# Performance work log

Measured on AMD Instinct MI355X. Metric: run time of the kernel, lower is better.

Reference implementation:

```python
import jax, jax.numpy as jnp
import numpy as np

B, N, C = 8, 4096, 1024
ATT_DIM = 512
M = 64  # num_outputs


def setup_inputs() -> dict:
    key = jax.random.key(0)
    k_x, k_w, k_b, k_av = jax.random.split(key, 4)
    x = jax.random.normal(k_x, (B, N, C), dtype=jnp.float32)
    # nn.Linear(input_dim, attention_dim): weight (att, C), bias (att,)
    lim = 1.0 / np.sqrt(C)
    W = jax.random.uniform(k_w, (ATT_DIM, C), dtype=jnp.float32, minval=-lim, maxval=lim)
    b = jax.random.uniform(k_b, (ATT_DIM,), dtype=jnp.float32, minval=-lim, maxval=lim)
    # torch.rand -> uniform [0,1)
    attention_vectors = jax.random.uniform(k_av, (M, ATT_DIM), dtype=jnp.float32)
    return {"x": x, "W": W, "b": b, "attention_vectors": attention_vectors}


def reference(x, W, b, attention_vectors):
    # linear projection: (B,N,C) @ (C,att) + bias -> (B,N,att)
    scores = jnp.einsum('bnc,dc->bnd', x, W) + b
    # learned-query attention logits: (B,M,N)
    logits = jnp.einsum('bnd,md->bmn', scores, attention_vectors)
    weights = jax.nn.softmax(logits, axis=-1)
    # pool original features: (B,M,N) @ (B,N,C) -> (B,M,C)
    return jnp.einsum('bmn,bnc->bmc', weights, x)
```

## Files before the change

kernel.cpp:

```cpp
#include <hip/hip_runtime.h>
#include <hip/hip_bf16.h>

#define Bn 8
#define Nn 4096
#define Cn 1024
#define Dn 512
#define Mn 64

typedef __hip_bfloat16 bf16;
typedef __attribute__((ext_vector_type(8))) short short8;
typedef __attribute__((ext_vector_type(4))) short short4x;
typedef __attribute__((ext_vector_type(4))) float f32x4;

#define MFMA16(a, b, c) __builtin_amdgcn_mfma_f32_16x16x32_bf16((a), (b), (c), 0, 0, 0)

__device__ inline short bfbits(float f) {
  union { bf16 b; short s; } u;
  u.b = __float2bfloat16(f);
  return u.s;
}
__device__ inline float bfval(short s) {
  union { short s; bf16 b; } u;
  u.s = s;
  return __bfloat162float(u.b);
}

__global__ __launch_bounds__(256) void prep_kernel(
    const float* __restrict__ W, const float* __restrict__ bias,
    const float* __restrict__ av, bf16* __restrict__ Vhi,
    bf16* __restrict__ Vlo, float* __restrict__ c0) {
  const int m = blockIdx.x;
  const int t = threadIdx.x;
  const int cl = t & 63, dg = t >> 6;
  const int c = blockIdx.y * 64 + cl;
  const float* wp = W + (size_t)(dg * 128) * Cn + c;
  const float* ap = av + m * Dn + dg * 128;
  float a0 = 0.f, a1 = 0.f, a2 = 0.f, a3 = 0.f;
#pragma unroll 8
  for (int i = 0; i < 128; i += 4) {
    a0 = fmaf(ap[i + 0], wp[(size_t)(i + 0) * Cn], a0);
    a1 = fmaf(ap[i + 1], wp[(size_t)(i + 1) * Cn], a1);
    a2 = fmaf(ap[i + 2], wp[(size_t)(i + 2) * Cn], a2);
    a3 = fmaf(ap[i + 3], wp[(size_t)(i + 3) * Cn], a3);
  }
  __shared__ float red[256];
  red[t] = (a0 + a1) + (a2 + a3);
  __syncthreads();
  const float v = red[cl] + red[cl + 64] + red[cl + 128] + red[cl + 192];
  if (dg == 0) {
    const bf16 hi = __float2bfloat16(v);
    Vhi[m * Cn + c] = hi;
    Vlo[m * Cn + c] = __float2bfloat16(v - __bfloat162float(hi));
  }
  if (blockIdx.y == 0) {
    __syncthreads();
    red[t] = av[m * Dn + t] * bias[t] + av[m * Dn + t + 256] * bias[t + 256];
    __syncthreads();
    if (t < 64) {
      float s = red[t] + red[t + 64] + red[t + 128] + red[t + 192];
#pragma unroll
      for (int off = 32; off > 0; off >>= 1) s += __shfl_down(s, off);
      if (t == 0) c0[m] = s;
    }
  }
}

__global__ __launch_bounds__(256, 2) void logits_sm_kernel(
    const float* __restrict__ x, const bf16* __restrict__ Vhi,
    const bf16* __restrict__ Vlo, const float* __restrict__ c0,
    bf16* __restrict__ wgt, float* __restrict__ Mp, float* __restrict__ Sp) {
  const int g = blockIdx.x;
  const int n0 = g * 64;
  const int b = blockIdx.y;
  const int t = threadIdx.x;
  const int w = t >> 6, lane = t & 63, lr = lane & 15, q = lane >> 4;

  const float* xrow = x + (size_t)(b * Nn + n0 + w * 16 + lr) * Cn + q * 8;
  const bf16* vh = Vhi + (size_t)lr * Cn + q * 8;
  const bf16* vl = Vlo + (size_t)lr * Cn + q * 8;

  f32x4 acc[4];
#pragma unroll
  for (int i = 0; i < 4; ++i) acc[i] = (f32x4){0.f, 0.f, 0.f, 0.f};

  float4 xa0[4], xa1[4], xb0[4], xb1[4], xc0[4], xc1[4];
#pragma unroll
  for (int s = 0; s < 4; ++s) {
    xa0[s] = *(const float4*)(xrow + s * 32);
    xa1[s] = *(const float4*)(xrow + s * 32 + 4);
    xb0[s] = *(const float4*)(xrow + 128 + s * 32);
    xb1[s] = *(const float4*)(xrow + 128 + s * 32 + 4);
    xc0[s] = xb0[s]; xc1[s] = xb1[s];
  }

  for (int kc = 0; kc < Cn; kc += 128) {
    if (kc + 256 < Cn) {
#pragma unroll
      for (int s = 0; s < 4; ++s) {
        xc0[s] = *(const float4*)(xrow + kc + 256 + s * 32);
        xc1[s] = *(const float4*)(xrow + kc + 256 + s * 32 + 4);
      }
    }
#pragma unroll
    for (int s = 0; s < 4; ++s) {
      const int kk = kc + s * 32;
      short8 a;
      a[0] = bfbits(xa0[s].x); a[1] = bfbits(xa0[s].y);
      a[2] = bfbits(xa0[s].z); a[3] = bfbits(xa0[s].w);
      a[4] = bfbits(xa1[s].x); a[5] = bfbits(xa1[s].y);
      a[6] = bfbits(xa1[s].z); a[7] = bfbits(xa1[s].w);
#pragma unroll
      for (int mt = 0; mt < 4; ++mt) {
        acc[mt] = MFMA16(a, *(const short8*)(vh + (size_t)(mt * 16) * Cn + kk), acc[mt]);
        acc[mt] = MFMA16(a, *(const short8*)(vl + (size_t)(mt * 16) * Cn + kk), acc[mt]);
      }
    }
#pragma unroll
    for (int s = 0; s < 4; ++s) {
      xa0[s] = xb0[s]; xa1[s] = xb1[s];
      xb0[s] = xc0[s]; xb1[s] = xc1[s];
    }
  }

  __shared__ float wredM[256];
  __shared__ float wredS[256];
  float rmax[4];
#pragma unroll
  for (int mt = 0; mt < 4; ++mt) {
    float r = fmaxf(fmaxf(acc[mt][0], acc[mt][1]), fmaxf(acc[mt][2], acc[mt][3]));
    r = fmaxf(r, __shfl_xor(r, 16));
    r = fmaxf(r, __shfl_xor(r, 32));
    rmax[mt] = r;
  }
  if (q == 0)
#pragma unroll
    for (int mt = 0; mt < 4; ++mt) wredM[w * 64 + mt * 16 + lr] = rmax[mt];
  __syncthreads();
  float vv[4][4];
#pragma unroll
  for (int mt = 0; mt < 4; ++mt) {
    const int m = mt * 16 + lr;
    const float mp = fmaxf(fmaxf(wredM[m], wredM[64 + m]),
                           fmaxf(wredM[128 + m], wredM[192 + m]));
    float s = 0.f;
#pragma unroll
    for (int r = 0; r < 4; ++r) {
      vv[mt][r] = __expf(acc[mt][r] - mp);
      s += vv[mt][r];
    }
    s += __shfl_xor(s, 16);
    s += __shfl_xor(s, 32);
    if (q == 0) wredS[w * 64 + m] = s;
  }
#pragma unroll
  for (int mt = 0; mt < 4; ++mt) {
    const int m = mt * 16 + lr;
    short4x o;
    o[0] = bfbits(vv[mt][0]); o[1] = bfbits(vv[mt][1]);
    o[2] = bfbits(vv[mt][2]); o[3] = bfbits(vv[mt][3]);
    *(short4x*)&wgt[(size_t)(b * Mn + m) * Nn + n0 + w * 16 + q * 4] = o;
  }
  __syncthreads();
  if (w == 0) {
    const int m = lane;
    const float mp = fmaxf(fmaxf(wredM[m], wredM[64 + m]),
                           fmaxf(wredM[128 + m], wredM[192 + m]));
    const float sp = wredS[m] + wredS[64 + m] + wredS[128 + m] + wredS[192 + m];
    Mp[((size_t)b * Mn + m) * 64 + g] = mp + c0[m];
    Sp[((size_t)b * Mn + m) * 64 + g] = sp;
  }
}

__global__ __launch_bounds__(256) void norm_kernel(
    bf16* __restrict__ wgt, const float* __restrict__ Mp,
    const float* __restrict__ Sp) {
  const int row = blockIdx.x;
  const int t = threadIdx.x;
  __shared__ float sMS[2];
  if (t < 64) {
    const float mp = Mp[(size_t)row * 64 + t];
    const float sp = Sp[(size_t)row * 64 + t];
    float M = mp;
#pragma unroll
    for (int off = 32; off > 0; off >>= 1) M = fmaxf(M, __shfl_xor(M, off));
    float e = __expf(mp - M) * sp;
#pragma unroll
    for (int off = 32; off > 0; off >>= 1) e += __shfl_xor(e, off);
    if (t == 0) { sMS[0] = M; sMS[1] = e; }
  }
  __syncthreads();
  const float M = sMS[0], inv = 1.f / sMS[1];
  const float sc = __expf(Mp[(size_t)row * 64 + (t >> 2)] - M) * inv;
  bf16* wp = wgt + (size_t)row * Nn + t * 16;
  short8 u0 = *(const short8*)(wp);
  short8 u1 = *(const short8*)(wp + 8);
  short8 o0, o1;
#pragma unroll
  for (int j = 0; j < 8; ++j) {
    o0[j] = bfbits(bfval(u0[j]) * sc);
    o1[j] = bfbits(bfval(u1[j]) * sc);
  }
  *(short8*)(wp) = o0;
  *(short8*)(wp + 8) = o1;
}

__global__ __launch_bounds__(256, 4) void pool_kernel(
    const float* __restrict__ x, const bf16* __restrict__ wgt,
    float* __restrict__ part) {
  const int cbase = blockIdx.x * 64;
  const int b = blockIdx.y;
  const int ks = blockIdx.z;
  const int t = threadIdx.x;
  __shared__ short XT[2][64][136];
  const int w = t >> 6, lane = t & 63, lr = lane & 15, q = lane >> 4;
  const int mh = (w & 1) * 32, ch = (w >> 1) * 32;
  f32x4 acc[2][2];
#pragma unroll
  for (int i = 0; i < 2; ++i)
#pragma unroll
    for (int j = 0; j < 2; ++j) acc[i][j] = (f32x4){0.f, 0.f, 0.f, 0.f};

  const int h = t & 15, g = t >> 4;
  const int swz = 8 * (h & 7);
  const int swzr0 = 8 * (((ch + lr) >> 2) & 7);
  const int swzr1 = 8 * (((ch + 16 + lr) >> 2) & 7);
  const int NQ = Nn / 8;
  const int kbase = ks * NQ;
  const float* xsrc = x + (size_t)b * Nn * Cn + (size_t)(kbase + 4 * g) * Cn + cbase + 4 * h;
  const bf16* wr0 = wgt + (size_t)(b * Mn + mh + lr) * Nn + kbase;
  const bf16* wr1 = wr0 + (size_t)16 * Nn;

  float4 pf[8];
#pragma unroll
  for (int i = 0; i < 4; ++i) {
    pf[i]     = *(const float4*)(xsrc + (size_t)i * Cn);
    pf[4 + i] = *(const float4*)(xsrc + (size_t)(64 + i) * Cn);
  }
#pragma unroll
  for (int blk = 0; blk < 2; ++blk) {
    const float4 r0 = pf[blk * 4 + 0], r1 = pf[blk * 4 + 1];
    const float4 r2 = pf[blk * 4 + 2], r3 = pf[blk * 4 + 3];
    const int kof = (blk * 64 + 4 * g) ^ swz;
    short4x v0, v1, v2, v3;
    v0[0] = bfbits(r0.x); v0[1] = bfbits(r1.x); v0[2] = bfbits(r2.x); v0[3] = bfbits(r3.x);
    v1[0] = bfbits(r0.y); v1[1] = bfbits(r1.y); v1[2] = bfbits(r2.y); v1[3] = bfbits(r3.y);
    v2[0] = bfbits(r0.z); v2[1] = bfbits(r1.z); v2[2] = bfbits(r2.z); v2[3] = bfbits(r3.z);
    v3[0] = bfbits(r0.w); v3[1] = bfbits(r1.w); v3[2] = bfbits(r2.w); v3[3] = bfbits(r3.w);
    *(short4x*)&XT[0][4 * h + 0][kof] = v0;
    *(short4x*)&XT[0][4 * h + 1][kof] = v1;
    *(short4x*)&XT[0][4 * h + 2][kof] = v2;
    *(short4x*)&XT[0][4 * h + 3][kof] = v3;
  }
#pragma unroll
  for (int i = 0; i < 4; ++i) {
    pf[i]     = *(const float4*)(xsrc + (size_t)(128 + i) * Cn);
    pf[4 + i] = *(const float4*)(xsrc + (size_t)(192 + i) * Cn);
  }

  int cur = 0;
  for (int kc = 0; kc < NQ; kc += 128, cur ^= 1) {
    __syncthreads();
    if (kc + 128 < NQ) {
#pragma unroll
      for (int blk = 0; blk < 2; ++blk) {
        const float4 r0 = pf[blk * 4 + 0], r1 = pf[blk * 4 + 1];
        const float4 r2 = pf[blk * 4 + 2], r3 = pf[blk * 4 + 3];
        const int kof = (blk * 64 + 4 * g) ^ swz;
        short4x v0, v1, v2, v3;
        v0[0] = bfbits(r0.x); v0[1] = bfbits(r1.x); v0[2] = bfbits(r2.x); v0[3] = bfbits(r3.x);
        v1[0] = bfbits(r0.y); v1[1] = bfbits(r1.y); v1[2] = bfbits(r2.y); v1[3] = bfbits(r3.y);
        v2[0] = bfbits(r0.z); v2[1] = bfbits(r1.z); v2[2] = bfbits(r2.z); v2[3] = bfbits(r3.z);
        v3[0] = bfbits(r0.w); v3[1] = bfbits(r1.w); v3[2] = bfbits(r2.w); v3[3] = bfbits(r3.w);
        *(short4x*)&XT[cur ^ 1][4 * h + 0][kof] = v0;
        *(short4x*)&XT[cur ^ 1][4 * h + 1][kof] = v1;
        *(short4x*)&XT[cur ^ 1][4 * h + 2][kof] = v2;
        *(short4x*)&XT[cur ^ 1][4 * h + 3][kof] = v3;
      }
      if (kc + 256 < NQ) {
#pragma unroll
        for (int i = 0; i < 4; ++i) {
          pf[i]     = *(const float4*)(xsrc + (size_t)(kc + 256 + i) * Cn);
          pf[4 + i] = *(const float4*)(xsrc + (size_t)(kc + 320 + i) * Cn);
        }
      }
    }
#pragma unroll
    for (int kk = 0; kk < 128; kk += 32) {
      const short8 a0 = *(const short8*)(wr0 + kc + kk + q * 8);
      const short8 a1 = *(const short8*)(wr1 + kc + kk + q * 8);
      const short8 b0 = *(const short8*)&XT[cur][ch + lr][(kk + q * 8) ^ swzr0];
      const short8 b1 = *(const short8*)&XT[cur][ch + 16 + lr][(kk + q * 8) ^ swzr1];
      acc[0][0] = MFMA16(a0, b0, acc[0][0]);
      acc[0][1] = MFMA16(a0, b1, acc[0][1]);
      acc[1][0] = MFMA16(a1, b0, acc[1][0]);
      acc[1][1] = MFMA16(a1, b1, acc[1][1]);
    }
  }
  float* pout = part + ((size_t)ks * Bn + b) * Mn * Cn;
#pragma unroll
  for (int mi = 0; mi < 2; ++mi)
#pragma unroll
    for (int ci = 0; ci < 2; ++ci) {
      const int m = mh + mi * 16 + q * 4;
      const int c = cbase + ch + ci * 16 + lr;
#pragma unroll
      for (int reg = 0; reg < 4; ++reg)
        pout[(size_t)(m + reg) * Cn + c] = acc[mi][ci][reg];
    }
}

__global__ __launch_bounds__(256) void reduce_kernel(
    const float* __restrict__ part, float* __restrict__ out) {
  const int i = blockIdx.x * 256 + threadIdx.x;
  const float4* p = (const float4*)part;
  const int S4 = (Bn * Mn * Cn) / 4;
  float4 o = (float4){0.f, 0.f, 0.f, 0.f};
#pragma unroll
  for (int j = 0; j < 8; ++j) {
    const float4 v = p[i + j * S4];
    o.x += v.x; o.y += v.y; o.z += v.z; o.w += v.w;
  }
  ((float4*)out)[i] = o;
}

extern "C" void kernel_launch(void* const* d_in, const int* in_sizes, int n_in,
                              void* d_out, int out_size, void* d_ws, size_t ws_size,
                              hipStream_t stream) {
  const float* x = (const float*)d_in[0];
  const float* W = (const float*)d_in[1];
  const float* bias = (const float*)d_in[2];
  const float* av = (const float*)d_in[3];
  float* out = (float*)d_out;
  char* ws = (char*)d_ws;

  bf16* Vhi = (bf16*)(ws + 0);
  bf16* Vlo = (bf16*)(ws + 131072);
  float* c0 = (float*)(ws + 262144);
  bf16* wgt = (bf16*)(ws + 263168);
  float* Mp = (float*)(ws + 4457472);
  float* Sp = (float*)(ws + 4588544);
  float* part = (float*)(ws + 4719616);

  prep_kernel<<<dim3(Mn, Cn / 64), 256, 0, stream>>>(W, bias, av, Vhi, Vlo, c0);
  logits_sm_kernel<<<dim3(Nn / 64, Bn), 256, 0, stream>>>(x, Vhi, Vlo, c0, wgt, Mp, Sp);
  norm_kernel<<<Bn * Mn, 256, 0, stream>>>(wgt, Mp, Sp);
  pool_kernel<<<dim3(Cn / 64, Bn, 8), 256, 0, stream>>>(x, wgt, part);
  reduce_kernel<<<(Bn * Mn * Cn) / 1024, 256, 0, stream>>>(part, out);
}
```

Baseline: 289.7 us.

## Stage V tiles in LDS and split softmax into separate fp32 logits pass

The logits kernel now cooperatively loads the bf16 hi/lo projection tiles into double-buffered shared memory instead of having every wave read them straight from global memory. The per-block partial softmax statistics and the rescaling pass are replaced by writing full fp32 logits (plus the bias term) to the workspace, followed by a standalone row-wise softmax kernel. This is meant to cut redundant global V traffic and simplify the epilogue. In exchange it writes and re-reads an 8 MB fp32 logits buffer, adds a barrier to every 64-wide K step, and reuses the logits workspace region for the pool partials.

```diff
diff --git a/kernel.cpp b/kernel.cpp
--- a/kernel.cpp
+++ b/kernel.cpp
@@ -18,11 +18,6 @@
   union { bf16 b; short s; } u;
   u.b = __float2bfloat16(f);
   return u.s;
-}
-__device__ inline float bfval(short s) {
-  union { short s; bf16 b; } u;
-  u.s = s;
-  return __bfloat162float(u.b);
 }
 
 __global__ __launch_bounds__(256) void prep_kernel(
@@ -65,45 +60,76 @@
   }
 }
 
-__global__ __launch_bounds__(256, 2) void logits_sm_kernel(
+__global__ __launch_bounds__(256, 2) void logits_kernel(
     const float* __restrict__ x, const bf16* __restrict__ Vhi,
     const bf16* __restrict__ Vlo, const float* __restrict__ c0,
-    bf16* __restrict__ wgt, float* __restrict__ Mp, float* __restrict__ Sp) {
-  const int g = blockIdx.x;
-  const int n0 = g * 64;
+    float* __restrict__ logits) {
+  const int n0 = blockIdx.x * 64;
   const int b = blockIdx.y;
   const int t = threadIdx.x;
+  __shared__ short VsH[2][64][72];
+  __shared__ short VsL[2][64][72];
   const int w = t >> 6, lane = t & 63, lr = lane & 15, q = lane >> 4;
 
   const float* xrow = x + (size_t)(b * Nn + n0 + w * 16 + lr) * Cn + q * 8;
-  const bf16* vh = Vhi + (size_t)lr * Cn + q * 8;
-  const bf16* vl = Vlo + (size_t)lr * Cn + q * 8;
+
+  const int vr = t >> 3, vs = (t & 7) * 8;
+  const bf16* vh0 = Vhi + (size_t)vr * Cn + vs;
+  const bf16* vh1 = vh0 + (size_t)32 * Cn;
+  const bf16* vl0 = Vlo + (size_t)vr * Cn + vs;
+  const bf16* vl1 = vl0 + (size_t)32 * Cn;
 
   f32x4 acc[4];
 #pragma unroll
   for (int i = 0; i < 4; ++i) acc[i] = (f32x4){0.f, 0.f, 0.f, 0.f};
 
-  float4 xa0[4], xa1[4], xb0[4], xb1[4], xc0[4], xc1[4];
-#pragma unroll
-  for (int s = 0; s < 4; ++s) {
+  short8 ph0 = *(const short8*)(vh0);
+  short8 ph1 = *(const short8*)(vh1);
+  short8 pl0 = *(const short8*)(vl0);
+  short8 pl1 = *(const short8*)(vl1);
+  *(short8*)&VsH[0][vr][vs] = ph0;
+  *(short8*)&VsH[0][vr + 32][vs] = ph1;
+  *(short8*)&VsL[0][vr][vs] = pl0;
+  *(short8*)&VsL[0][vr + 32][vs] = pl1;
+  ph0 = *(const short8*)(vh0 + 64);
+  ph1 = *(const short8*)(vh1 + 64);
+  pl0 = *(const short8*)(vl0 + 64);
+  pl1 = *(const short8*)(vl1 + 64);
+
+  float4 xa0[2], xa1[2], xb0[2], xb1[2], xc0[2], xc1[2];
+#pragma unroll
+  for (int s = 0; s < 2; ++s) {
     xa0[s] = *(const float4*)(xrow + s * 32);
     xa1[s] = *(const float4*)(xrow + s * 32 + 4);
-    xb0[s] = *(const float4*)(xrow + 128 + s * 32);
-    xb1[s] = *(const float4*)(xrow + 128 + s * 32 + 4);
+    xb0[s] = *(const float4*)(xrow + 64 + s * 32);
+    xb1[s] = *(const float4*)(xrow + 64 + s * 32 + 4);
     xc0[s] = xb0[s]; xc1[s] = xb1[s];
   }
 
-  for (int kc = 0; kc < Cn; kc += 128) {
-    if (kc + 256 < Cn) {
-#pragma unroll
-      for (int s = 0; s < 4; ++s) {
-        xc0[s] = *(const float4*)(xrow + kc + 256 + s * 32);
-        xc1[s] = *(const float4*)(xrow + kc + 256 + s * 32 + 4);
-      }
-    }
-#pragma unroll
-    for (int s = 0; s < 4; ++s) {
-      const int kk = kc + s * 32;
+  int cur = 0;
+  for (int kc = 0; kc < Cn; kc += 64, cur ^= 1) {
+    __syncthreads();
+    if (kc + 64 < Cn) {
+      *(short8*)&VsH[cur ^ 1][vr][vs] = ph0;
+      *(short8*)&VsH[cur ^ 1][vr + 32][vs] = ph1;
+      *(short8*)&VsL[cur ^ 1][vr][vs] = pl0;
+      *(short8*)&VsL[cur ^ 1][vr + 32][vs] = pl1;
+      if (kc + 128 < Cn) {
+        ph0 = *(const short8*)(vh0 + kc + 128);
+        ph1 = *(const short8*)(vh1 + kc + 128);
+        pl0 = *(const short8*)(vl0 + kc + 128);
+        pl1 = *(const short8*)(vl1 + kc + 128);
+      }
+    }
+    if (kc + 128 < Cn) {
+#pragma unroll
+      for (int s = 0; s < 2; ++s) {
+        xc0[s] = *(const float4*)(xrow + kc + 128 + s * 32);
+        xc1[s] = *(const float4*)(xrow + kc + 128 + s * 32 + 4);
+      }
+    }
+#pragma unroll
+    for (int s = 0; s < 2; ++s) {
       short8 a;
       a[0] = bfbits(xa0[s].x); a[1] = bfbits(xa0[s].y);
       a[2] = bfbits(xa0[s].z); a[3] = bfbits(xa0[s].w);
@@ -111,97 +137,60 @@
       a[6] = bfbits(xa1[s].z); a[7] = bfbits(xa1[s].w);
 #pragma unroll
       for (int mt = 0; mt < 4; ++mt) {
-        acc[mt] = MFMA16(a, *(const short8*)(vh + (size_t)(mt * 16) * Cn + kk), acc[mt]);
-        acc[mt] = MFMA16(a, *(const short8*)(vl + (size_t)(mt * 16) * Cn + kk), acc[mt]);
-      }
-    }
-#pragma unroll
-    for (int s = 0; s < 4; ++s) {
+        acc[mt] = MFMA16(a, *(const short8*)&VsH[cur][mt * 16 + lr][s * 32 + q * 8], acc[mt]);
+        acc[mt] = MFMA16(a, *(const short8*)&VsL[cur][mt * 16 + lr][s * 32 + q * 8], acc[mt]);
+      }
+    }
+#pragma unroll
+    for (int s = 0; s < 2; ++s) {
       xa0[s] = xb0[s]; xa1[s] = xb1[s];
       xb0[s] = xc0[s]; xb1[s] = xc1[s];
     }
   }
-
-  __shared__ float wredM[256];
-  __shared__ float wredS[256];
-  float rmax[4];
-#pragma unroll
-  for (int mt = 0; mt < 4; ++mt) {
-    float r = fmaxf(fmaxf(acc[mt][0], acc[mt][1]), fmaxf(acc[mt][2], acc[mt][3]));
-    r = fmaxf(r, __shfl_xor(r, 16));
-    r = fmaxf(r, __shfl_xor(r, 32));
-    rmax[mt] = r;
-  }
-  if (q == 0)
-#pragma unroll
-    for (int mt = 0; mt < 4; ++mt) wredM[w * 64 + mt * 16 + lr] = rmax[mt];
-  __syncthreads();
-  float vv[4][4];
 #pragma unroll
   for (int mt = 0; mt < 4; ++mt) {
     const int m = mt * 16 + lr;
-    const float mp = fmaxf(fmaxf(wredM[m], wredM[64 + m]),
-                           fmaxf(wredM[128 + m], wredM[192 + m]));
-    float s = 0.f;
-#pragma unroll
-    for (int r = 0; r < 4; ++r) {
-      vv[mt][r] = __expf(acc[mt][r] - mp);
-      s += vv[mt][r];
-    }
-    s += __shfl_xor(s, 16);
-    s += __shfl_xor(s, 32);
-    if (q == 0) wredS[w * 64 + m] = s;
-  }
-#pragma unroll
-  for (int mt = 0; mt < 4; ++mt) {
-    const int m = mt * 16 + lr;
-    short4x o;
-    o[0] = bfbits(vv[mt][0]); o[1] = bfbits(vv[mt][1]);
-    o[2] = bfbits(vv[mt][2]); o[3] = bfbits(vv[mt][3]);
-    *(short4x*)&wgt[(size_t)(b * Mn + m) * Nn + n0 + w * 16 + q * 4] = o;
-  }
-  __syncthreads();
-  if (w == 0) {
-    const int m = lane;
-    const float mp = fmaxf(fmaxf(wredM[m], wredM[64 + m]),
-                           fmaxf(wredM[128 + m], wredM[192 + m]));
-    const float sp = wredS[m] + wredS[64 + m] + wredS[128 + m] + wredS[192 + m];
-    Mp[((size_t)b * Mn + m) * 64 + g] = mp + c0[m];
-    Sp[((size_t)b * Mn + m) * 64 + g] = sp;
-  }
-}
-
-__global__ __launch_bounds__(256) void norm_kernel(
-    bf16* __restrict__ wgt, const float* __restrict__ Mp,
-    const float* __restrict__ Sp) {
+    const float bb = c0[m];
+    float4 o;
+    o.x = acc[mt][0] + bb; o.y = acc[mt][1] + bb;
+    o.z = acc[mt][2] + bb; o.w = acc[mt][3] + bb;
+    *(float4*)&logits[(size_t)(b * Mn + m) * Nn + n0 + w * 16 + q * 4] = o;
+  }
+}
+
+__global__ __launch_bounds__(256) void softmax_kernel(
+    const float* __restrict__ logits, bf16* __restrict__ wgt) {
   const int row = blockIdx.x;
   const int t = threadIdx.x;
-  __shared__ float sMS[2];
-  if (t < 64) {
-    const float mp = Mp[(size_t)row * 64 + t];
-    const float sp = Sp[(size_t)row * 64 + t];
-    float M = mp;
-#pragma unroll
-    for (int off = 32; off > 0; off >>= 1) M = fmaxf(M, __shfl_xor(M, off));
-    float e = __expf(mp - M) * sp;
-#pragma unroll
-    for (int off = 32; off > 0; off >>= 1) e += __shfl_xor(e, off);
-    if (t == 0) { sMS[0] = M; sMS[1] = e; }
-  }
+  const float* L = logits + (size_t)row * Nn;
+  float v[16];
+  float mx = -3.4e38f;
+#pragma unroll
+  for (int i = 0; i < 16; ++i) {
+    v[i] = L[t + 256 * i];
+    mx = fmaxf(mx, v[i]);
+  }
+#pragma unroll
+  for (int off = 32; off > 0; off >>= 1) mx = fmaxf(mx, __shfl_down(mx, off));
+  __shared__ float sred[4];
+  if ((t & 63) == 0) sred[t >> 6] = mx;
   __syncthreads();
-  const float M = sMS[0], inv = 1.f / sMS[1];
-  const float sc = __expf(Mp[(size_t)row * 64 + (t >> 2)] - M) * inv;
-  bf16* wp = wgt + (size_t)row * Nn + t * 16;
-  short8 u0 = *(const short8*)(wp);
-  short8 u1 = *(const short8*)(wp + 8);
-  short8 o0, o1;
-#pragma unroll
-  for (int j = 0; j < 8; ++j) {
-    o0[j] = bfbits(bfval(u0[j]) * sc);
-    o1[j] = bfbits(bfval(u1[j]) * sc);
-  }
-  *(short8*)(wp) = o0;
-  *(short8*)(wp + 8) = o1;
+  mx = fmaxf(fmaxf(sred[0], sred[1]), fmaxf(sred[2], sred[3]));
+  float sum = 0.f;
+#pragma unroll
+  for (int i = 0; i < 16; ++i) {
+    v[i] = __expf(v[i] - mx);
+    sum += v[i];
+  }
+#pragma unroll
+  for (int off = 32; off > 0; off >>= 1) sum += __shfl_down(sum, off);
+  __syncthreads();
+  if ((t & 63) == 0) sred[t >> 6] = sum;
+  __syncthreads();
+  const float inv = 1.f / (sred[0] + sred[1] + sred[2] + sred[3]);
+#pragma unroll
+  for (int i = 0; i < 16; ++i)
+    wgt[(size_t)row * Nn + t + 256 * i] = __float2bfloat16(v[i] * inv);
 }
 
 __global__ __launch_bounds__(256, 4) void pool_kernel(
@@ -337,13 +326,12 @@
   bf16* Vlo = (bf16*)(ws + 131072);
   float* c0 = (float*)(ws + 262144);
   bf16* wgt = (bf16*)(ws + 263168);
-  float* Mp = (float*)(ws + 4457472);
-  float* Sp = (float*)(ws + 4588544);
-  float* part = (float*)(ws + 4719616);
+  float* logits = (float*)(ws + 4457472);
+  float* part = (float*)(ws + 4457472);
 
   prep_kernel<<<dim3(Mn, Cn / 64), 256, 0, stream>>>(W, bias, av, Vhi, Vlo, c0);
-  logits_sm_kernel<<<dim3(Nn / 64, Bn), 256, 0, stream>>>(x, Vhi, Vlo, c0, wgt, Mp, Sp);
-  norm_kernel<<<Bn * Mn, 256, 0, stream>>>(wgt, Mp, Sp);
+  logits_kernel<<<dim3(Nn / 64, Bn), 256, 0, stream>>>(x, Vhi, Vlo, c0, logits);
+  softmax_kernel<<<Bn * Mn, 256, 0, stream>>>(logits, wgt);
   pool_kernel<<<dim3(Cn / 64, Bn, 8), 256, 0, stream>>>(x, wgt, part);
   reduce_kernel<<<(Bn * Mn * Cn) / 1024, 256, 0, stream>>>(part, out);
 }
```

Result: faster. 254.8 us (-12.0%).
